# Performance work log

Hardware: AMD Instinct MI355X
Metric: run time of the kernel (lower is better)

The kernel has to match this reference:

```python
import jax, jax.numpy as jnp
import numpy as np

N, D, H, DF = 2048, 1024, 16, 4096
DK = D // H
EPS = 1e-5


def layernorm(x, g, b):
    mu = jnp.mean(x, axis=-1, keepdims=True)
    var = jnp.mean((x - mu) ** 2, axis=-1, keepdims=True)
    return (x - mu) * jax.lax.rsqrt(var + EPS) * g + b


def setup_inputs() -> dict:
    key = jax.random.key(0)
    ks = jax.random.split(key, 8)
    s = 0.02
    return {
        "X": jax.random.normal(ks[0], (N, D), dtype=jnp.float32),
        "Wqkv": jax.random.normal(ks[1], (2 * D, D), dtype=jnp.float32) * s,
        "W1": jax.random.normal(ks[2], (DF, D), dtype=jnp.float32) * s,
        "b1": jnp.zeros((DF,), dtype=jnp.float32),
        "W2": jax.random.normal(ks[3], (D, DF), dtype=jnp.float32) * s,
        "b2": jnp.zeros((D,), dtype=jnp.float32),
        "g1": jnp.ones((D,), dtype=jnp.float32),
        "be1": jnp.zeros((D,), dtype=jnp.float32),
        "g2": jnp.ones((D,), dtype=jnp.float32),
        "be2": jnp.zeros((D,), dtype=jnp.float32),
    }


def reference(X, Wqkv, W1, b1, W2, b2, g1, be1, g2, be2):
    # shared-QK multi-head attention (Q == K), no bias
    qkv = X @ Wqkv.T                      # [N, 2D]
    qk, v = jnp.split(qkv, 2, axis=-1)    # [N, D] each
    qk = qk.reshape(N, H, DK)
    v = v.reshape(N, H, DK)
    scale = DK ** 0.5
    scores = jnp.einsum('nhd,mhd->hnm', qk, qk) / scale  # [H, N, N]
    att = jax.nn.softmax(scores, axis=-1)
    attn_out = jnp.einsum('hnm,mhd->nhd', att, v).reshape(N, D)
    # residual + LN, FFN (dropout is identity in eval), residual + LN
    h = layernorm(X + attn_out, g1, be1)
    ffn = jax.nn.relu(h @ W1.T + b1) @ W2.T + b2
    return layernorm(h + ffn, g2, be2)
```

## Files before the change

kernel.cpp:

```cpp
#include <hip/hip_runtime.h>
#include <stdint.h>


#define NTOK 2048
#define DMODEL 1024
#define NHEAD 16
#define DHEAD 64
#define DFF 4096

typedef __attribute__((ext_vector_type(8))) short short8;
typedef __attribute__((ext_vector_type(4))) short short4v;
typedef __attribute__((ext_vector_type(4))) float f32x4;

__device__ __forceinline__ float fexp2(float x) { return __builtin_amdgcn_exp2f(x); }

__device__ __forceinline__ short f2b(float f) {
  union { float f; unsigned u; } v; v.f = f;
  unsigned r = v.u + 0x7fffu + ((v.u >> 16) & 1u);
  return (short)(r >> 16);
}

__device__ __forceinline__ void gload_lds16(const void* g, void* l) {
  __builtin_amdgcn_global_load_lds((const __attribute__((address_space(1))) void*)g,
                                   (__attribute__((address_space(3))) void*)l,
                                   16, 0, 0);
}

__global__ void cast_all(const float* __restrict__ s0, short* __restrict__ d0, int n0,
                         const float* __restrict__ s1, short* __restrict__ d1, int n1,
                         const float* __restrict__ s2, short* __restrict__ d2, int n2,
                         const float* __restrict__ s3, short* __restrict__ d3, int n3) {
  int i = blockIdx.x * blockDim.x + threadIdx.x;
  const float* s; short* d; int j = i;
  if (j < n0) { s = s0; d = d0; }
  else { j -= n0;
    if (j < n1) { s = s1; d = d1; }
    else { j -= n1;
      if (j < n2) { s = s2; d = d2; }
      else { j -= n2; if (j >= n3) return; s = s3; d = d3; }
    }
  }
  const float4* p = (const float4*)(s + (size_t)j * 8);
  float4 a = p[0], b = p[1];
  short8 o;
  o[0] = f2b(a.x); o[1] = f2b(a.y); o[2] = f2b(a.z); o[3] = f2b(a.w);
  o[4] = f2b(b.x); o[5] = f2b(b.y); o[6] = f2b(b.z); o[7] = f2b(b.w);
  *(short8*)(d + (size_t)j * 8) = o;
}

template<int BM, int BN, int WR, int WC, bool BF16OUT, bool BIAS, bool RELU>
__launch_bounds__(WR * WC * 64)
__global__ void gemm_bt(const short* __restrict__ A, const short* __restrict__ B,
                        const float* __restrict__ bias,
                        float* __restrict__ Cf, short* __restrict__ Cb,
                        int M, int N, int K, int lda, int ldb, int kstep) {
  constexpr int BK = 64;
  constexpr int THREADS = WR * WC * 64;
  constexpr int ACH = (BM * (BK / 8)) / THREADS;
  constexpr int BCH = (BN * (BK / 8)) / THREADS;
  __shared__ short As[2][BM * BK];
  __shared__ short Bs[2][BN * BK];
  const int t = threadIdx.x;
  const int l = t & 63;
  const int w = t >> 6;
  const int wr = w / WC, wc = w % WC;
  const int lr = l & 15, lg = l >> 4;
  const int m0 = blockIdx.y * BM, n0 = blockIdx.x * BN;
  const int koff = blockIdx.z * kstep;
  A += koff; B += koff;
  Cf += (size_t)blockIdx.z * M * N;

  auto stage = [&](int b, int k0) {
#pragma unroll
    for (int i = 0; i < ACH; ++i) {
      const int ci = i * THREADS + t;
      const int r = ci >> 3, c = ci & 7;
      const int cs = c ^ (r & 7);
      gload_lds16(A + (size_t)(m0 + r) * lda + k0 + cs * 8,
                  &As[b][(size_t)(i * THREADS + w * 64) * 8]);
    }
#pragma unroll
    for (int i = 0; i < BCH; ++i) {
      const int ci = i * THREADS + t;
      const int r = ci >> 3, c = ci & 7;
      const int cs = c ^ (r & 7);
      gload_lds16(B + (size_t)(n0 + r) * ldb + k0 + cs * 8,
                  &Bs[b][(size_t)(i * THREADS + w * 64) * 8]);
    }
  };

  f32x4 acc[4][4] = {};
  const int nIter = K / BK;
  stage(0, 0);
  __syncthreads();
  for (int it = 0; it < nIter; ++it) {
    const int cur = it & 1;
    if (it + 1 < nIter) stage(cur ^ 1, (it + 1) * BK);
#pragma unroll
    for (int kk = 0; kk < 2; ++kk) {
      short8 a[4], b[4];
#pragma unroll
      for (int m = 0; m < 4; ++m) {
        const int r = wr * 64 + m * 16 + lr;
        a[m] = *(const short8*)(&As[cur][r * BK + (((kk * 4 + lg) ^ (r & 7)) * 8)]);
      }
#pragma unroll
      for (int n = 0; n < 4; ++n) {
        const int r = wc * 64 + n * 16 + lr;
        b[n] = *(const short8*)(&Bs[cur][r * BK + (((kk * 4 + lg) ^ (r & 7)) * 8)]);
      }
#pragma unroll
      for (int m = 0; m < 4; ++m)
#pragma unroll
        for (int n = 0; n < 4; ++n)
          acc[m][n] = __builtin_amdgcn_mfma_f32_16x16x32_bf16(a[m], b[n], acc[m][n], 0, 0, 0);
    }
    __syncthreads();
  }
#pragma unroll
  for (int n = 0; n < 4; ++n) {
    const int col = n0 + wc * 64 + n * 16 + lr;
    const float bv = BIAS ? bias[col] : 0.0f;
#pragma unroll
    for (int m = 0; m < 4; ++m) {
#pragma unroll
      for (int r = 0; r < 4; ++r) {
        const int row = m0 + wr * 64 + m * 16 + lg * 4 + r;
        float v = acc[m][n][r] + bv;
        if (RELU) v = fmaxf(v, 0.0f);
        if (BF16OUT) Cb[(size_t)row * N + col] = f2b(v);
        else         Cf[(size_t)row * N + col] = v;
      }
    }
  }
}

__global__ void transpose_v(const short* __restrict__ src, short* __restrict__ dst) {
  __shared__ short tile[64][65];
  const int bx = blockIdx.x * 64;
  const int by = blockIdx.y * 64;
  const int t = threadIdx.x;
  const int tx = t & 63, ty = t >> 6;
#pragma unroll
  for (int i = 0; i < 64; i += 4)
    tile[ty + i][tx] = src[(size_t)(by + ty + i) * 2048 + 1024 + bx + tx];
  __syncthreads();
#pragma unroll
  for (int i = 0; i < 64; i += 4)
    dst[(size_t)(bx + ty + i) * 2048 + by + tx] = tile[tx][ty + i];
}

__launch_bounds__(256, 2)
__global__ void flash_attn(const short* __restrict__ qk, const short* __restrict__ vt,
                           float* __restrict__ O) {
  const int t = threadIdx.x;
  const int l = t & 63, w = t >> 6;
  const int lr = l & 15, lg = l >> 4;
  const int h = blockIdx.y;
  const int qb = blockIdx.x;
  __shared__ short Ks[2][64 * 64];
  __shared__ short Vs[2][64 * 64];
  __shared__ short Pl[4][16][72];
  const float C2 = 0.18033688011112042f;

  const int qrow = qb * 64 + w * 16 + lr;
  short8 aq[2];
#pragma unroll
  for (int f = 0; f < 2; ++f)
    aq[f] = *(const short8*)(qk + (size_t)qrow * 2048 + h * 64 + f * 32 + lg * 8);

  f32x4 o[4] = {};
  float mrun = -1e30f, lrun = 0.0f;

  auto stage = [&](int b, int kt) {
#pragma unroll
    for (int i = 0; i < 2; ++i) {
      const int chunk = i * 256 + w * 64 + l;
      const int r = chunk >> 3, c = chunk & 7;
      const int cs = c ^ (r & 7);
      gload_lds16(qk + (size_t)(kt * 64 + r) * 2048 + h * 64 + cs * 8,
                  &Ks[b][(size_t)(i * 256 + w * 64) * 8]);
    }
#pragma unroll
    for (int i = 0; i < 2; ++i) {
      const int chunk = i * 256 + w * 64 + l;
      const int r = chunk >> 3, c = chunk & 7;
      const int cs = c ^ (r & 7);
      gload_lds16(vt + (size_t)(h * 64 + r) * 2048 + kt * 64 + cs * 8,
                  &Vs[b][(size_t)(i * 256 + w * 64) * 8]);
    }
  };

  stage(0, 0);
  __syncthreads();

#pragma unroll 1
  for (int kt = 0; kt < 32; ++kt) {
    const int cur = kt & 1;
    if (kt + 1 < 32) stage(cur ^ 1, kt + 1);

    f32x4 s[4] = {};
#pragma unroll
    for (int f = 0; f < 2; ++f) {
      short8 kf[4];
#pragma unroll
      for (int n = 0; n < 4; ++n) {
        const int r = n * 16 + lr;
        kf[n] = *(const short8*)(&Ks[cur][r * 64 + (((f * 4 + lg) ^ (lr & 7)) * 8)]);
      }
#pragma unroll
      for (int n = 0; n < 4; ++n)
        s[n] = __builtin_amdgcn_mfma_f32_16x16x32_bf16(kf[n], aq[f], s[n], 0, 0, 0);
    }
    float m0 = fmaxf(fmaxf(s[0][0], s[0][1]), fmaxf(s[0][2], s[0][3]));
    float m1 = fmaxf(fmaxf(s[1][0], s[1][1]), fmaxf(s[1][2], s[1][3]));
    float m2 = fmaxf(fmaxf(s[2][0], s[2][1]), fmaxf(s[2][2], s[2][3]));
    float m3 = fmaxf(fmaxf(s[3][0], s[3][1]), fmaxf(s[3][2], s[3][3]));
    float tm = fmaxf(fmaxf(m0, m1), fmaxf(m2, m3));
    tm = fmaxf(tm, __shfl_xor(tm, 16));
    tm = fmaxf(tm, __shfl_xor(tm, 32));
    const float mnew = fmaxf(mrun, tm);
    const float corr = fexp2((mrun - mnew) * C2);
    mrun = mnew;
    float p[4][4];
#pragma unroll
    for (int n = 0; n < 4; ++n)
#pragma unroll
      for (int r = 0; r < 4; ++r)
        p[n][r] = fexp2((s[n][r] - mnew) * C2);
    float q0 = (p[0][0] + p[0][1]) + (p[0][2] + p[0][3]);
    float q1 = (p[1][0] + p[1][1]) + (p[1][2] + p[1][3]);
    float q2 = (p[2][0] + p[2][1]) + (p[2][2] + p[2][3]);
    float q3 = (p[3][0] + p[3][1]) + (p[3][2] + p[3][3]);
    float ps = (q0 + q1) + (q2 + q3);
    ps += __shfl_xor(ps, 16);
    ps += __shfl_xor(ps, 32);
    lrun = lrun * corr + ps;
    f32x4 cov;
#pragma unroll
    for (int r = 0; r < 4; ++r)
      cov[r] = __shfl(corr, lg * 4 + r);
#pragma unroll
    for (int n = 0; n < 4; ++n)
      o[n] *= cov;
#pragma unroll
    for (int n = 0; n < 4; ++n) {
      uint2 wv;
      wv.x = ((unsigned)(unsigned short)f2b(p[n][1]) << 16) | (unsigned short)f2b(p[n][0]);
      wv.y = ((unsigned)(unsigned short)f2b(p[n][3]) << 16) | (unsigned short)f2b(p[n][2]);
      *(uint2*)&Pl[w][lr][n * 16 + lg * 4] = wv;
    }
#pragma unroll
    for (int f = 0; f < 2; ++f) {
      short8 ap = *(const short8*)&Pl[w][lr][f * 32 + lg * 8];
      short8 vf[4];
#pragma unroll
      for (int n = 0; n < 4; ++n) {
        const int r = n * 16 + lr;
        vf[n] = *(const short8*)(&Vs[cur][r * 64 + (((f * 4 + lg) ^ (lr & 7)) * 8)]);
      }
#pragma unroll
      for (int n = 0; n < 4; ++n)
        o[n] = __builtin_amdgcn_mfma_f32_16x16x32_bf16(ap, vf[n], o[n], 0, 0, 0);
    }
    __syncthreads();
  }

  f32x4 inv;
#pragma unroll
  for (int r = 0; r < 4; ++r)
    inv[r] = 1.0f / __shfl(lrun, lg * 4 + r);
#pragma unroll
  for (int n = 0; n < 4; ++n)
#pragma unroll
    for (int r = 0; r < 4; ++r)
      O[(size_t)(qb * 64 + w * 16 + lg * 4 + r) * 1024 + h * 64 + n * 16 + lr] = o[n][r] * inv[r];
}

__launch_bounds__(256)
__global__ void add_ln(const float* __restrict__ A, const float* __restrict__ B0,
                       const float* __restrict__ B1, const float* __restrict__ bias,
                       const float* __restrict__ g, const float* __restrict__ be,
                       float* __restrict__ outf, short* __restrict__ outb) {
  const int row = blockIdx.x;
  const int t = threadIdx.x;
  const size_t base = (size_t)row * 1024 + t * 4;
  float4 a = *(const float4*)(A + base);
  float4 b = *(const float4*)(B0 + base);
  float4 s; s.x = a.x + b.x; s.y = a.y + b.y; s.z = a.z + b.z; s.w = a.w + b.w;
  if (B1) {
    float4 c = *(const float4*)(B1 + base);
    s.x += c.x; s.y += c.y; s.z += c.z; s.w += c.w;
  }
  if (bias) {
    float4 c = *(const float4*)(bias + t * 4);
    s.x += c.x; s.y += c.y; s.z += c.z; s.w += c.w;
  }
  float sum = s.x + s.y + s.z + s.w;
  float sq  = s.x * s.x + s.y * s.y + s.z * s.z + s.w * s.w;
#pragma unroll
  for (int d = 32; d > 0; d >>= 1) {
    sum += __shfl_down(sum, d);
    sq  += __shfl_down(sq, d);
  }
  __shared__ float red[8];
  const int w = t >> 6, l = t & 63;
  if (l == 0) { red[w] = sum; red[4 + w] = sq; }
  __syncthreads();
  sum = red[0] + red[1] + red[2] + red[3];
  sq  = red[4] + red[5] + red[6] + red[7];
  const float mu = sum * (1.0f / 1024.0f);
  const float rstd = rsqrtf(sq * (1.0f / 1024.0f) - mu * mu + 1e-5f);
  float4 gv = *(const float4*)(g + t * 4);
  float4 bv = *(const float4*)(be + t * 4);
  float4 o;
  o.x = (s.x - mu) * rstd * gv.x + bv.x;
  o.y = (s.y - mu) * rstd * gv.y + bv.y;
  o.z = (s.z - mu) * rstd * gv.z + bv.z;
  o.w = (s.w - mu) * rstd * gv.w + bv.w;
  *(float4*)(outf + base) = o;
  if (outb) {
    short4v ob; ob.x = f2b(o.x); ob.y = f2b(o.y); ob.z = f2b(o.z); ob.w = f2b(o.w);
    *(short4v*)(outb + base) = ob;
  }
}

extern "C" void kernel_launch(void* const* d_in, const int* in_sizes, int n_in,
                              void* d_out, int out_size, void* d_ws, size_t ws_size,
                              hipStream_t stream) {
  const float* X    = (const float*)d_in[0];
  const float* Wqkv = (const float*)d_in[1];
  const float* W1   = (const float*)d_in[2];
  const float* b1   = (const float*)d_in[3];
  const float* W2   = (const float*)d_in[4];
  const float* b2   = (const float*)d_in[5];
  const float* g1   = (const float*)d_in[6];
  const float* be1  = (const float*)d_in[7];
  const float* g2   = (const float*)d_in[8];
  const float* be2  = (const float*)d_in[9];

  char* ws = (char*)d_ws;
  const size_t MiB = 1u << 20;
  short*  W1b   = (short*)(ws + 0 * MiB);
  short*  W2b   = (short*)(ws + 8 * MiB);
  float*  h     = (float*)(ws + 16 * MiB);
  short*  hb    = (short*)(ws + 24 * MiB);
  short*  qkvb  = (short*)(ws + 28 * MiB);
  short*  y1b   = (short*)(ws + 28 * MiB);
  short*  vt    = (short*)(ws + 36 * MiB);
  float*  attn  = (float*)(ws + 44 * MiB);
  float*  P0    = (float*)(ws + 44 * MiB);
  float*  P1    = P0 + (size_t)NTOK * DMODEL;
  short*  Xb    = (short*)(ws + 52 * MiB);
  short*  Wqkvb = (short*)(ws + 56 * MiB);

  cast_all<<<6144, 256, 0, stream>>>(X, Xb, NTOK * DMODEL / 8,
                                     Wqkv, Wqkvb, 2 * DMODEL * DMODEL / 8,
                                     W1, W1b, DFF * DMODEL / 8,
                                     W2, W2b, DMODEL * DFF / 8);

  {
    dim3 grid(2 * DMODEL / 128, NTOK / 128, 1);
    gemm_bt<128, 128, 2, 2, true, false, false><<<grid, 256, 0, stream>>>(
        Xb, Wqkvb, nullptr, nullptr, qkvb, NTOK, 2 * DMODEL, DMODEL, DMODEL, DMODEL, 0);
  }
  {
    dim3 grid(DMODEL / 64, NTOK / 64);
    transpose_v<<<grid, 256, 0, stream>>>(qkvb, vt);
  }
  {
    dim3 grid(NTOK / 64, NHEAD);
    flash_attn<<<grid, 256, 0, stream>>>(qkvb, vt, attn);
  }
  add_ln<<<NTOK, 256, 0, stream>>>(X, attn, nullptr, nullptr, g1, be1, h, hb);
  {
    dim3 grid(DFF / 128, NTOK / 128, 1);
    gemm_bt<128, 128, 2, 2, true, true, true><<<grid, 256, 0, stream>>>(
        hb, W1b, b1, nullptr, y1b, NTOK, DFF, DMODEL, DMODEL, DMODEL, 0);
  }
  {
    dim3 grid(DMODEL / 128, NTOK / 128, 2);
    gemm_bt<128, 128, 2, 2, false, false, false><<<grid, 256, 0, stream>>>(
        y1b, W2b, nullptr, P0, nullptr, NTOK, DMODEL, 2048, DFF, DFF, 2048);
  }
  add_ln<<<NTOK, 256, 0, stream>>>(h, P0, P1, b2, g2, be2, (float*)d_out, nullptr);
}
```

Measured before the change: 251.1 us.

## Shrink GEMM M-tile to 64, add setprio and lazy rescale in flash attention

The GEMM template is generalised so per-wave fragment counts follow from the tile shape. All three GEMMs now use 64x128 tiles with a minimum of 3 blocks per CU, giving more blocks for the 256-CU part at the cost of less reuse per tile. In flash attention, MFMA sections get raised wave priority, and the output rescale is skipped when no running max rises. The skip saves exp and shuffle work but adds a wave-wide vote.

```diff
diff --git a/kernel.cpp b/kernel.cpp
--- a/kernel.cpp
+++ b/kernel.cpp
@@ -49,7 +49,7 @@
 }
 
 template<int BM, int BN, int WR, int WC, bool BF16OUT, bool BIAS, bool RELU>
-__launch_bounds__(WR * WC * 64)
+__launch_bounds__(WR * WC * 64, 3)
 __global__ void gemm_bt(const short* __restrict__ A, const short* __restrict__ B,
                         const float* __restrict__ bias,
                         float* __restrict__ Cf, short* __restrict__ Cb,
@@ -58,6 +58,8 @@
   constexpr int THREADS = WR * WC * 64;
   constexpr int ACH = (BM * (BK / 8)) / THREADS;
   constexpr int BCH = (BN * (BK / 8)) / THREADS;
+  constexpr int MR = BM / (WR * 16);
+  constexpr int NR = BN / (WC * 16);
   __shared__ short As[2][BM * BK];
   __shared__ short Bs[2][BN * BK];
   const int t = threadIdx.x;
@@ -89,7 +91,7 @@
     }
   };
 
-  f32x4 acc[4][4] = {};
+  f32x4 acc[MR][NR] = {};
   const int nIter = K / BK;
   stage(0, 0);
   __syncthreads();
@@ -98,34 +100,34 @@
     if (it + 1 < nIter) stage(cur ^ 1, (it + 1) * BK);
 #pragma unroll
     for (int kk = 0; kk < 2; ++kk) {
-      short8 a[4], b[4];
-#pragma unroll
-      for (int m = 0; m < 4; ++m) {
-        const int r = wr * 64 + m * 16 + lr;
+      short8 a[MR], b[NR];
+#pragma unroll
+      for (int m = 0; m < MR; ++m) {
+        const int r = wr * (BM / WR) + m * 16 + lr;
         a[m] = *(const short8*)(&As[cur][r * BK + (((kk * 4 + lg) ^ (r & 7)) * 8)]);
       }
 #pragma unroll
-      for (int n = 0; n < 4; ++n) {
-        const int r = wc * 64 + n * 16 + lr;
+      for (int n = 0; n < NR; ++n) {
+        const int r = wc * (BN / WC) + n * 16 + lr;
         b[n] = *(const short8*)(&Bs[cur][r * BK + (((kk * 4 + lg) ^ (r & 7)) * 8)]);
       }
 #pragma unroll
-      for (int m = 0; m < 4; ++m)
-#pragma unroll
-        for (int n = 0; n < 4; ++n)
+      for (int m = 0; m < MR; ++m)
+#pragma unroll
+        for (int n = 0; n < NR; ++n)
           acc[m][n] = __builtin_amdgcn_mfma_f32_16x16x32_bf16(a[m], b[n], acc[m][n], 0, 0, 0);
     }
     __syncthreads();
   }
 #pragma unroll
-  for (int n = 0; n < 4; ++n) {
-    const int col = n0 + wc * 64 + n * 16 + lr;
+  for (int n = 0; n < NR; ++n) {
+    const int col = n0 + wc * (BN / WC) + n * 16 + lr;
     const float bv = BIAS ? bias[col] : 0.0f;
 #pragma unroll
-    for (int m = 0; m < 4; ++m) {
+    for (int m = 0; m < MR; ++m) {
 #pragma unroll
       for (int r = 0; r < 4; ++r) {
-        const int row = m0 + wr * 64 + m * 16 + lg * 4 + r;
+        const int row = m0 + wr * (BM / WR) + m * 16 + lg * 4 + r;
         float v = acc[m][n][r] + bv;
         if (RELU) v = fmaxf(v, 0.0f);
         if (BF16OUT) Cb[(size_t)row * N + col] = f2b(v);
@@ -200,6 +202,7 @@
     if (kt + 1 < 32) stage(cur ^ 1, kt + 1);
 
     f32x4 s[4] = {};
+    __builtin_amdgcn_s_setprio(1);
 #pragma unroll
     for (int f = 0; f < 2; ++f) {
       short8 kf[4];
@@ -212,6 +215,7 @@
       for (int n = 0; n < 4; ++n)
         s[n] = __builtin_amdgcn_mfma_f32_16x16x32_bf16(kf[n], aq[f], s[n], 0, 0, 0);
     }
+    __builtin_amdgcn_s_setprio(0);
     float m0 = fmaxf(fmaxf(s[0][0], s[0][1]), fmaxf(s[0][2], s[0][3]));
     float m1 = fmaxf(fmaxf(s[1][0], s[1][1]), fmaxf(s[1][2], s[1][3]));
     float m2 = fmaxf(fmaxf(s[2][0], s[2][1]), fmaxf(s[2][2], s[2][3]));
@@ -219,15 +223,25 @@
     float tm = fmaxf(fmaxf(m0, m1), fmaxf(m2, m3));
     tm = fmaxf(tm, __shfl_xor(tm, 16));
     tm = fmaxf(tm, __shfl_xor(tm, 32));
-    const float mnew = fmaxf(mrun, tm);
-    const float corr = fexp2((mrun - mnew) * C2);
-    mrun = mnew;
+    float corrv = 1.0f;
+    if (__any(tm > mrun)) {
+      const float mnew = fmaxf(mrun, tm);
+      corrv = fexp2((mrun - mnew) * C2);
+      mrun = mnew;
+      f32x4 cov;
+#pragma unroll
+      for (int r = 0; r < 4; ++r)
+        cov[r] = __shfl(corrv, lg * 4 + r);
+#pragma unroll
+      for (int n = 0; n < 4; ++n)
+        o[n] *= cov;
+    }
     float p[4][4];
 #pragma unroll
     for (int n = 0; n < 4; ++n)
 #pragma unroll
       for (int r = 0; r < 4; ++r)
-        p[n][r] = fexp2((s[n][r] - mnew) * C2);
+        p[n][r] = fexp2((s[n][r] - mrun) * C2);
     float q0 = (p[0][0] + p[0][1]) + (p[0][2] + p[0][3]);
     float q1 = (p[1][0] + p[1][1]) + (p[1][2] + p[1][3]);
     float q2 = (p[2][0] + p[2][1]) + (p[2][2] + p[2][3]);
@@ -235,14 +249,7 @@
     float ps = (q0 + q1) + (q2 + q3);
     ps += __shfl_xor(ps, 16);
     ps += __shfl_xor(ps, 32);
-    lrun = lrun * corr + ps;
-    f32x4 cov;
-#pragma unroll
-    for (int r = 0; r < 4; ++r)
-      cov[r] = __shfl(corr, lg * 4 + r);
-#pragma unroll
-    for (int n = 0; n < 4; ++n)
-      o[n] *= cov;
+    lrun = lrun * corrv + ps;
 #pragma unroll
     for (int n = 0; n < 4; ++n) {
       uint2 wv;
@@ -250,6 +257,7 @@
       wv.y = ((unsigned)(unsigned short)f2b(p[n][3]) << 16) | (unsigned short)f2b(p[n][2]);
       *(uint2*)&Pl[w][lr][n * 16 + lg * 4] = wv;
     }
+    __builtin_amdgcn_s_setprio(1);
 #pragma unroll
     for (int f = 0; f < 2; ++f) {
       short8 ap = *(const short8*)&Pl[w][lr][f * 32 + lg * 8];
@@ -263,6 +271,7 @@
       for (int n = 0; n < 4; ++n)
         o[n] = __builtin_amdgcn_mfma_f32_16x16x32_bf16(ap, vf[n], o[n], 0, 0, 0);
     }
+    __builtin_amdgcn_s_setprio(0);
     __syncthreads();
   }
 
@@ -360,8 +369,8 @@
                                      W2, W2b, DMODEL * DFF / 8);
 
   {
-    dim3 grid(2 * DMODEL / 128, NTOK / 128, 1);
-    gemm_bt<128, 128, 2, 2, true, false, false><<<grid, 256, 0, stream>>>(
+    dim3 grid(2 * DMODEL / 128, NTOK / 64, 1);
+    gemm_bt<64, 128, 2, 2, true, false, false><<<grid, 256, 0, stream>>>(
         Xb, Wqkvb, nullptr, nullptr, qkvb, NTOK, 2 * DMODEL, DMODEL, DMODEL, DMODEL, 0);
   }
   {
@@ -374,13 +383,13 @@
   }
   add_ln<<<NTOK, 256, 0, stream>>>(X, attn, nullptr, nullptr, g1, be1, h, hb);
   {
-    dim3 grid(DFF / 128, NTOK / 128, 1);
-    gemm_bt<128, 128, 2, 2, true, true, true><<<grid, 256, 0, stream>>>(
+    dim3 grid(DFF / 128, NTOK / 64, 1);
+    gemm_bt<64, 128, 2, 2, true, true, true><<<grid, 256, 0, stream>>>(
         hb, W1b, b1, nullptr, y1b, NTOK, DFF, DMODEL, DMODEL, DMODEL, 0);
   }
   {
-    dim3 grid(DMODEL / 128, NTOK / 128, 2);
-    gemm_bt<128, 128, 2, 2, false, false, false><<<grid, 256, 0, stream>>>(
+    dim3 grid(DMODEL / 128, NTOK / 64, 2);
+    gemm_bt<64, 128, 2, 2, false, false, false><<<grid, 256, 0, stream>>>(
         y1b, W2b, nullptr, P0, nullptr, NTOK, DMODEL, 2048, DFF, DFF, 2048);
   }
   add_ln<<<NTOK, 256, 0, stream>>>(h, P0, P1, b2, g2, be2, (float*)d_out, nullptr);
```

Result: faster. 243.9 us (-2.9%).
